# Performance work log

Measured on AMD Instinct MI355X. Metric: run time of the kernel, lower is better.

Reference implementation:

```python
import jax, jax.numpy as jnp
import numpy as np

VOCAB, D = 32000, 1024
EPS = 1e-5

def setup_inputs() -> dict:
    key = jax.random.key(0)
    k1, k2, k3, k4 = jax.random.split(key, 4)
    patch_embeddings = jax.random.normal(k1, (16, 256, D), dtype=jnp.float32)
    text_prototypes = jax.random.normal(k2, (VOCAB, D), dtype=jnp.float32) * 0.02
    # nn.Linear(d, d): weight [d, d], bias [d]
    lim = 1.0 / np.sqrt(D)
    W = jax.random.uniform(k3, (D, D), minval=-lim, maxval=lim, dtype=jnp.float32)
    b = jax.random.uniform(k4, (D,), minval=-lim, maxval=lim, dtype=jnp.float32)
    gamma = jnp.ones((D,), dtype=jnp.float32)
    beta = jnp.zeros((D,), dtype=jnp.float32)
    return {"patch_embeddings": patch_embeddings, "text_prototypes": text_prototypes,
            "W": W, "b": b, "gamma": gamma, "beta": beta}

def _layer_norm(x, gamma, beta):
    mu = jnp.mean(x, axis=-1, keepdims=True)
    var = jnp.mean(jnp.square(x - mu), axis=-1, keepdims=True)
    return (x - mu) * jax.lax.rsqrt(var + EPS) * gamma + beta

def reference(patch_embeddings, text_prototypes, W, b, gamma, beta):
    # similarities: [B, P, V]
    sims = jnp.einsum('bpd,vd->bpv', patch_embeddings, text_prototypes)
    attn = jax.nn.softmax(sims, axis=-1)
    reprogrammed = jnp.einsum('bpv,vd->bpd', attn, text_prototypes)
    transformed = jnp.einsum('bpd,ed->bpe', reprogrammed, W) + b
    return _layer_norm(patch_embeddings + transformed, gamma, beta)
```

## Files before the change

kernel.cpp:

```cpp
#include <hip/hip_runtime.h>
#include <hip/hip_bf16.h>
#include <cstdint>
#include <cstddef>

#define D_DIM 1024
#define VOCAB 32000
#define ROWS  4096

typedef __attribute__((ext_vector_type(8))) short bf16x8;
typedef __attribute__((ext_vector_type(4))) float f32x4;
typedef __attribute__((ext_vector_type(4))) int   i32x4;
typedef __attribute__((ext_vector_type(8))) int   i32x8;

static __device__ __forceinline__ i32x8 cat8(i32x4 lo, i32x4 hi) {
  return __builtin_shufflevector(lo, hi, 0, 1, 2, 3, 4, 5, 6, 7);
}

static __device__ __forceinline__ unsigned short f2bf(float f) {
  union { float f; unsigned int u; } c; c.f = f;
  unsigned int u = c.u;
  u += 0x7fffu + ((u >> 16) & 1u);
  return (unsigned short)(u >> 16);
}

static __device__ __forceinline__ int pk8(float a, float b) {
  return __builtin_amdgcn_cvt_pk_fp8_f32(a, b, 0, false);
}

static __device__ __forceinline__ void gload_lds16(const void* g, void* s) {
  __builtin_amdgcn_global_load_lds(
      (const __attribute__((address_space(1))) uint32_t*)(g),
      (__attribute__((address_space(3))) uint32_t*)(s), 16, 0, 0);
}

__global__ void k_cvt(const float* __restrict__ src, short* __restrict__ dst, int n4) {
  int i = blockIdx.x * 256 + threadIdx.x;
  if (i < n4) {
    float4 v = *(const float4*)(src + (size_t)i * 4);
    ushort4 u;
    u.x = f2bf(v.x); u.y = f2bf(v.y); u.z = f2bf(v.z); u.w = f2bf(v.w);
    *(ushort4*)(dst + (size_t)i * 4) = u;
  }
}

__global__ void k_cvt_q8(const float* __restrict__ src, uint8_t* __restrict__ dst) {
  int i = blockIdx.x * 256 + threadIdx.x;
  float4 a = *(const float4*)(src + (size_t)i * 8);
  float4 b = *(const float4*)(src + (size_t)i * 8 + 4);
  uint2 o;
  o.x = (pk8(a.x, a.y) & 0xffff) | (pk8(a.z, a.w) << 16);
  o.y = (pk8(b.x, b.y) & 0xffff) | (pk8(b.z, b.w) << 16);
  *(uint2*)(dst + (size_t)i * 8) = o;
}

__global__ void k_prep_K8(const float* __restrict__ src, uint8_t* __restrict__ kb,
                          uint8_t* __restrict__ kt, int R, int C) {
  __shared__ uint8_t tile[64][68];
  int t  = threadIdx.x;
  int r0 = blockIdx.x * 64;
  int c0 = blockIdx.y * 64;
  int lr = t >> 4;
  int lc = (t & 15) * 4;
#pragma unroll
  for (int i = 0; i < 4; ++i) {
    int r = lr + 16 * i;
    float4 v = *(const float4*)(src + (size_t)(r0 + r) * C + c0 + lc);
    unsigned p = (pk8(v.x * 64.f, v.y * 64.f) & 0xffff) | (pk8(v.z * 64.f, v.w * 64.f) << 16);
    *(unsigned*)&tile[r][lc] = p;
    *(unsigned*)(kb + (size_t)(r0 + r) * C + c0 + lc) = p;
  }
  __syncthreads();
#pragma unroll
  for (int i = 0; i < 4; ++i) {
    int c = lr + 16 * i;
    unsigned p = tile[lc + 0][c] | (tile[lc + 1][c] << 8) |
                 (tile[lc + 2][c] << 16) | ((unsigned)tile[lc + 3][c] << 24);
    *(unsigned*)(kt + (size_t)(c0 + c) * R + r0 + lc) = p;
  }
}

#define PS1 272
#define G1NT 8
__global__ __launch_bounds__(512, 1) void k_g1(
    const uint8_t* __restrict__ A,
    const uint8_t* __restrict__ B,
    uint8_t* __restrict__ Pout, float* __restrict__ den)
{
  __shared__ uint8_t smem[147456];

  int tid  = threadIdx.x;
  int wave = tid >> 6;
  int lane = tid & 63;
  int quad = lane >> 4;
  int t16  = lane & 15;
  int wm = wave >> 2;
  int wn = wave & 3;

  int swz = (blockIdx.x & 7) * 500 + (blockIdx.x >> 3);
  int nt  = swz >> 5;
  int mt  = swz & 31;
  long mBase = (long)mt * 128;
  long nBase = (long)nt * 256;

  const uint8_t* Ab = A + (size_t)mBase * D_DIM;
  const uint8_t* Bb = B + (size_t)nBase * D_DIM;
  int lrow = lane >> 3;
  int lcol = ((lane & 7) ^ lrow) * 16;

  f32x4 acc[4][4];
#pragma unroll
  for (int i = 0; i < 4; ++i)
#pragma unroll
    for (int j = 0; j < 4; ++j) acc[i][j] = (f32x4){0.f, 0.f, 0.f, 0.f};

  int sw  = t16 & 7;
  int co0 = (((quad << 1) ^ sw) << 4);
  const int SC1 = 0x7F7F7F7F;

  auto STAGE = [&](int slot, int t) {
    uint8_t* As = &smem[slot * 49152];
    uint8_t* Bs = As + 16384;
    int kk = t * 128;
#pragma unroll
    for (int g = 0; g < 2; ++g) {
      int r0 = wave * 16 + g * 8;
      gload_lds16(Ab + (size_t)(r0 + lrow) * D_DIM + kk + lcol, As + r0 * 128);
    }
#pragma unroll
    for (int g = 0; g < 4; ++g) {
      int r0 = wave * 32 + g * 8;
      gload_lds16(Bb + (size_t)(r0 + lrow) * D_DIM + kk + lcol, Bs + r0 * 128);
    }
  };

  STAGE(0, 0);
  STAGE(1, 1);

  for (int t = 0; t < G1NT; ++t) {
    if (t + 1 < G1NT)
      asm volatile("s_waitcnt vmcnt(6)\n\ts_barrier" ::: "memory");
    else
      asm volatile("s_waitcnt vmcnt(0)\n\ts_barrier" ::: "memory");

    if (t + 2 < G1NT) STAGE((t + 2) % 3, t + 2);

    const uint8_t* As = &smem[(t % 3) * 49152];
    const uint8_t* Bs = As + 16384;
    i32x8 af[4], bfr[4];
#pragma unroll
    for (int mi = 0; mi < 4; ++mi) {
      const uint8_t* rp = &As[(wm * 64 + mi * 16 + t16) * 128];
      af[mi] = cat8(*(const i32x4*)(rp + co0), *(const i32x4*)(rp + (co0 ^ 16)));
    }
#pragma unroll
    for (int ni = 0; ni < 4; ++ni) {
      const uint8_t* rp = &Bs[(wn * 64 + ni * 16 + t16) * 128];
      bfr[ni] = cat8(*(const i32x4*)(rp + co0), *(const i32x4*)(rp + (co0 ^ 16)));
    }
    __builtin_amdgcn_s_setprio(1);
#pragma unroll
    for (int mi = 0; mi < 4; ++mi)
#pragma unroll
      for (int ni = 0; ni < 4; ++ni)
        acc[mi][ni] = __builtin_amdgcn_mfma_scale_f32_16x16x128_f8f6f4(
            af[mi], bfr[ni], acc[mi][ni], 0, 0, 0, SC1, 0, SC1);
    __builtin_amdgcn_s_setprio(0);
  }

  __syncthreads();
  float rsum[4][4];
#pragma unroll
  for (int mi = 0; mi < 4; ++mi)
#pragma unroll
    for (int r = 0; r < 4; ++r) rsum[mi][r] = 0.f;
#pragma unroll
  for (int mi = 0; mi < 4; ++mi) {
    int rloc = wm * 64 + mi * 16 + quad * 4;
#pragma unroll
    for (int ni = 0; ni < 4; ++ni) {
      int cloc = wn * 64 + ni * 16 + t16;
#pragma unroll
      for (int r = 0; r < 4; ++r) {
        float e = __expf(acc[mi][ni][r] * 0.015625f);
        smem[(rloc + r) * PS1 + cloc] = (uint8_t)pk8(e, e);
        rsum[mi][r] += e;
      }
    }
  }
#pragma unroll
  for (int mi = 0; mi < 4; ++mi)
#pragma unroll
    for (int r = 0; r < 4; ++r) {
      float s = rsum[mi][r];
      s += __shfl_xor(s, 1);
      s += __shfl_xor(s, 2);
      s += __shfl_xor(s, 4);
      s += __shfl_xor(s, 8);
      if (t16 == 0)
        atomicAdd(&den[mBase + wm * 64 + mi * 16 + quad * 4 + r], s);
    }
  __syncthreads();
  int rr  = tid >> 4;
  int c16 = (tid & 15) * 16;
#pragma unroll
  for (int i = 0; i < 4; ++i) {
    int row = i * 32 + rr;
    i32x4 v = *(const i32x4*)&smem[row * PS1 + c16];
    __builtin_nontemporal_store(v, (i32x4*)&Pout[(size_t)(mBase + row) * VOCAB + nBase + c16]);
  }
}

#define G2NT 125
__global__ __launch_bounds__(512, 1) void k_g2(
    const uint8_t* __restrict__ P, const uint8_t* __restrict__ KT,
    float* __restrict__ n0, float* __restrict__ n1)
{
  __shared__ uint8_t smem[147456];

  int tid  = threadIdx.x;
  int wave = tid >> 6;
  int lane = tid & 63;
  int quad = lane >> 4;
  int t16  = lane & 15;
  int wm = wave >> 2;
  int wn = wave & 3;

  int bid = blockIdx.x;
  int dt  = bid & 3;
  int zz  = (bid >> 2) & 1;
  int mt  = bid >> 3;
  long mBase = (long)mt * 128;
  long dBase = (long)dt * 256;
  int  k0    = zz * 16000;

  const uint8_t* Ab = P  + (size_t)mBase * VOCAB + k0;
  const uint8_t* Bb = KT + (size_t)dBase * VOCAB + k0;
  int lrow = lane >> 3;
  int lcol = ((lane & 7) ^ lrow) * 16;

  f32x4 acc[4][4];
#pragma unroll
  for (int i = 0; i < 4; ++i)
#pragma unroll
    for (int j = 0; j < 4; ++j) acc[i][j] = (f32x4){0.f, 0.f, 0.f, 0.f};

  int sw  = t16 & 7;
  int co0 = (((quad << 1) ^ sw) << 4);
  const int SC1 = 0x7F7F7F7F;

  auto STAGE = [&](int slot, int t) {
    uint8_t* As = &smem[slot * 49152];
    uint8_t* Bs = As + 16384;
    long kk = (long)t * 128;
#pragma unroll
    for (int g = 0; g < 2; ++g) {
      int r0 = wave * 16 + g * 8;
      gload_lds16(Ab + (size_t)(r0 + lrow) * VOCAB + kk + lcol, As + r0 * 128);
    }
#pragma unroll
    for (int g = 0; g < 4; ++g) {
      int r0 = wave * 32 + g * 8;
      gload_lds16(Bb + (size_t)(r0 + lrow) * VOCAB + kk + lcol, Bs + r0 * 128);
    }
  };

  STAGE(0, 0);
  STAGE(1, 1);

  for (int t = 0; t < G2NT; ++t) {
    if (t + 1 < G2NT)
      asm volatile("s_waitcnt vmcnt(6)\n\ts_barrier" ::: "memory");
    else
      asm volatile("s_waitcnt vmcnt(0)\n\ts_barrier" ::: "memory");

    if (t + 2 < G2NT) STAGE((t + 2) % 3, t + 2);

    const uint8_t* As = &smem[(t % 3) * 49152];
    const uint8_t* Bs = As + 16384;
    i32x8 af[4], bfr[4];
#pragma unroll
    for (int mi = 0; mi < 4; ++mi) {
      const uint8_t* rp = &As[(wm * 64 + mi * 16 + t16) * 128];
      af[mi] = cat8(*(const i32x4*)(rp + co0), *(const i32x4*)(rp + (co0 ^ 16)));
    }
#pragma unroll
    for (int ni = 0; ni < 4; ++ni) {
      const uint8_t* rp = &Bs[(wn * 64 + ni * 16 + t16) * 128];
      bfr[ni] = cat8(*(const i32x4*)(rp + co0), *(const i32x4*)(rp + (co0 ^ 16)));
    }
    __builtin_amdgcn_s_setprio(1);
#pragma unroll
    for (int mi = 0; mi < 4; ++mi)
#pragma unroll
      for (int ni = 0; ni < 4; ++ni)
        acc[mi][ni] = __builtin_amdgcn_mfma_scale_f32_16x16x128_f8f6f4(
            af[mi], bfr[ni], acc[mi][ni], 0, 0, 0, SC1, 0, SC1);
    __builtin_amdgcn_s_setprio(0);
  }

  float* outp = zz ? n1 : n0;
#pragma unroll
  for (int mi = 0; mi < 4; ++mi) {
    long row = mBase + wm * 64 + mi * 16 + quad * 4;
#pragma unroll
    for (int ni = 0; ni < 4; ++ni) {
      long col = dBase + wn * 64 + ni * 16 + t16;
#pragma unroll
      for (int r = 0; r < 4; ++r)
        outp[(size_t)(row + r) * D_DIM + col] = acc[mi][ni][r];
    }
  }
}

__global__ __launch_bounds__(256) void k_gemm_bf(
    const short* __restrict__ A, int lda,
    const short* __restrict__ B, int ldb, int Kdim,
    const float* __restrict__ bias, const float* __restrict__ resid,
    float* __restrict__ Cout)
{
  __shared__ short smem[16384];
  short* As = smem;
  short* Bs = smem + 8192;

  int tid  = threadIdx.x;
  int wave = tid >> 6;
  int lane = tid & 63;
  int quad = lane >> 4;
  int t16  = lane & 15;
  int wy = wave >> 1, wx = wave & 1;

  long mBase = (long)blockIdx.y * 128;
  long nBase = (long)blockIdx.x * 128;

  const short* Ab = A + (size_t)mBase * lda;
  const short* Bb = B + (size_t)nBase * ldb;
  int lrow = lane >> 3;
  int lcol = ((lane & 7) ^ lrow) * 8;

  f32x4 acc[4][4];
#pragma unroll
  for (int i = 0; i < 4; ++i)
#pragma unroll
    for (int j = 0; j < 4; ++j) acc[i][j] = (f32x4){0.f, 0.f, 0.f, 0.f};

  int sw = t16 & 7;

  for (int kk = 0; kk < Kdim; kk += 64) {
#pragma unroll
    for (int i = 0; i < 4; ++i) {
      int row = wave * 32 + i * 8;
      gload_lds16(Ab + (size_t)(row + lrow) * lda + kk + lcol, &As[row * 64]);
      gload_lds16(Bb + (size_t)(row + lrow) * ldb + kk + lcol, &Bs[row * 64]);
    }
    __syncthreads();
#pragma unroll
    for (int kc = 0; kc < 8; kc += 4) {
      bf16x8 af[4], bfr[4];
#pragma unroll
      for (int mi = 0; mi < 4; ++mi)
        af[mi] = *(const bf16x8*)&As[(wy * 64 + mi * 16 + t16) * 64 +
                                     (((kc + quad) ^ sw) << 3)];
#pragma unroll
      for (int ni = 0; ni < 4; ++ni)
        bfr[ni] = *(const bf16x8*)&Bs[(wx * 64 + ni * 16 + t16) * 64 +
                                      (((kc + quad) ^ sw) << 3)];
#pragma unroll
      for (int mi = 0; mi < 4; ++mi)
#pragma unroll
        for (int ni = 0; ni < 4; ++ni)
          acc[mi][ni] = __builtin_amdgcn_mfma_f32_16x16x32_bf16(af[mi], bfr[ni],
                                                                acc[mi][ni], 0, 0, 0);
    }
    __syncthreads();
  }

#pragma unroll
  for (int mi = 0; mi < 4; ++mi) {
    long row = mBase + wy * 64 + mi * 16 + quad * 4;
#pragma unroll
    for (int ni = 0; ni < 4; ++ni) {
      long col = nBase + wx * 64 + ni * 16 + t16;
#pragma unroll
      for (int r = 0; r < 4; ++r) {
        size_t idx = (size_t)(row + r) * 1024 + col;
        Cout[idx] = acc[mi][ni][r] + bias[col] + resid[idx];
      }
    }
  }
}

__global__ void k_div(const float* __restrict__ n0, const float* __restrict__ n1,
                      const float* __restrict__ den, short* __restrict__ out) {
  int i = (blockIdx.x * 256 + threadIdx.x) * 4;
  float4 a = *(const float4*)(n0 + i);
  float4 b = *(const float4*)(n1 + i);
  float inv = 0.015625f / den[i >> 10];
  ushort4 u;
  u.x = f2bf((a.x + b.x) * inv); u.y = f2bf((a.y + b.y) * inv);
  u.z = f2bf((a.z + b.z) * inv); u.w = f2bf((a.w + b.w) * inv);
  *(ushort4*)(out + i) = u;
}

__global__ __launch_bounds__(256) void k_ln(const float* __restrict__ x,
                                            const float* __restrict__ gamma,
                                            const float* __restrict__ beta,
                                            float* __restrict__ out) {
  __shared__ float s_sum[4], s_sq[4];
  int row = blockIdx.x;
  int tid = threadIdx.x;
  const float* xr = x + (size_t)row * 1024;
  float4 v = *(const float4*)(xr + tid * 4);
  float s = v.x + v.y + v.z + v.w;
  float q = v.x * v.x + v.y * v.y + v.z * v.z + v.w * v.w;
#pragma unroll
  for (int off = 32; off >= 1; off >>= 1) {
    s += __shfl_down(s, off);
    q += __shfl_down(q, off);
  }
  int wv = tid >> 6;
  if ((tid & 63) == 0) { s_sum[wv] = s; s_sq[wv] = q; }
  __syncthreads();
  float tot  = s_sum[0] + s_sum[1] + s_sum[2] + s_sum[3];
  float totq = s_sq[0] + s_sq[1] + s_sq[2] + s_sq[3];
  float mu   = tot * (1.0f / 1024.0f);
  float var  = totq * (1.0f / 1024.0f) - mu * mu;
  float rstd = rsqrtf(var + 1e-5f);
  float4 g = *(const float4*)(gamma + tid * 4);
  float4 b = *(const float4*)(beta + tid * 4);
  float4 o;
  o.x = (v.x - mu) * rstd * g.x + b.x;
  o.y = (v.y - mu) * rstd * g.y + b.y;
  o.z = (v.z - mu) * rstd * g.z + b.z;
  o.w = (v.w - mu) * rstd * g.w + b.w;
  *(float4*)(out + (size_t)row * 1024 + tid * 4) = o;
}

extern "C" void kernel_launch(void* const* d_in, const int* in_sizes, int n_in,
                              void* d_out, int out_size, void* d_ws, size_t ws_size,
                              hipStream_t stream) {
  const float* patch = (const float*)d_in[0];
  const float* proto = (const float*)d_in[1];
  const float* W     = (const float*)d_in[2];
  const float* bvec  = (const float*)d_in[3];
  const float* gamma = (const float*)d_in[4];
  const float* beta  = (const float*)d_in[5];
  float* out = (float*)d_out;

  char* ws = (char*)d_ws;
  size_t off = 0;
  uint8_t* Q8  = (uint8_t*)(ws + off); off += (size_t)ROWS * D_DIM;
  uint8_t* Kb8 = (uint8_t*)(ws + off); off += (size_t)VOCAB * D_DIM;
  uint8_t* KT8 = (uint8_t*)(ws + off); off += (size_t)VOCAB * D_DIM;
  short*   Wb  = (short*)(ws + off);   off += (size_t)D_DIM * D_DIM * 2;
  short*   Rb  = (short*)(ws + off);   off += (size_t)ROWS * D_DIM * 2;
  uint8_t* P8  = (uint8_t*)(ws + off); off += (size_t)ROWS * VOCAB;
  float*   num = (float*)(ws + off);   off += (size_t)ROWS * D_DIM * 4;
  float*   den = (float*)(ws + off);   off += (size_t)ROWS * 4;
  float*   pre = (float*)P8;
  float*   nz0 = (float*)Kb8;
  float*   nz1 = num;

  hipMemsetAsync(den, 0, ROWS * sizeof(float), stream);

  k_cvt_q8<<<ROWS * D_DIM / 8 / 256, 256, 0, stream>>>(patch, Q8);
  k_cvt<<<D_DIM * D_DIM / 4 / 256, 256, 0, stream>>>(W, Wb, D_DIM * D_DIM / 4);
  k_prep_K8<<<dim3(VOCAB / 64, D_DIM / 64), 256, 0, stream>>>(proto, Kb8, KT8, VOCAB, D_DIM);

  k_g1<<<4000, 512, 0, stream>>>(Q8, Kb8, P8, den);

  k_g2<<<256, 512, 0, stream>>>(P8, KT8, nz0, nz1);

  k_div<<<ROWS * D_DIM / 4 / 256, 256, 0, stream>>>(nz0, nz1, den, Rb);

  k_gemm_bf<<<dim3(D_DIM / 128, ROWS / 128), 256, 0, stream>>>(
      Rb, D_DIM, Wb, D_DIM, D_DIM, bvec, patch, pre);

  k_ln<<<ROWS, 256, 0, stream>>>(pre, gamma, beta, out);
}
```

Before: 634.9 us.

## Enlarge GEMM tiles to 256x256, double-buffer, and split g2 K five ways

Both fp8 GEMM kernels move from 128x256 to 256x256 block tiles with 8 MFMA column fragments per wave, which raises data reuse per LDS load. The K loop changes from a triple-buffered to a double-buffered LDS pipeline, with an explicit barrier before each refill. The second GEMM now splits K into five chunks over 320 blocks instead of two chunks over 256, to fill the GPU better. Four of the chunks accumulate through float atomics into buffers that are zeroed by an extra memset, and the divide kernel sums three partial buffers. The cost is more accumulator registers, atomic traffic, the extra memset and a shallower prefetch.

```diff
diff --git a/kernel.cpp b/kernel.cpp
--- a/kernel.cpp
+++ b/kernel.cpp
@@ -81,25 +81,25 @@
 
 #define PS1 272
 #define G1NT 8
-__global__ __launch_bounds__(512, 1) void k_g1(
+__global__ __launch_bounds__(512, 2) void k_g1(
     const uint8_t* __restrict__ A,
     const uint8_t* __restrict__ B,
     uint8_t* __restrict__ Pout, float* __restrict__ den)
 {
-  __shared__ uint8_t smem[147456];
+  __shared__ uint8_t smem[131072];
 
   int tid  = threadIdx.x;
   int wave = tid >> 6;
   int lane = tid & 63;
   int quad = lane >> 4;
   int t16  = lane & 15;
-  int wm = wave >> 2;
-  int wn = wave & 3;
-
-  int swz = (blockIdx.x & 7) * 500 + (blockIdx.x >> 3);
-  int nt  = swz >> 5;
-  int mt  = swz & 31;
-  long mBase = (long)mt * 128;
+  int wm = wave >> 1;
+  int wn = wave & 1;
+
+  int swz = (blockIdx.x & 7) * 250 + (blockIdx.x >> 3);
+  int nt  = swz >> 4;
+  int mt  = swz & 15;
+  long mBase = (long)mt * 256;
   long nBase = (long)nt * 256;
 
   const uint8_t* Ab = A + (size_t)mBase * D_DIM;
@@ -107,23 +107,23 @@
   int lrow = lane >> 3;
   int lcol = ((lane & 7) ^ lrow) * 16;
 
-  f32x4 acc[4][4];
+  f32x4 acc[4][8];
 #pragma unroll
   for (int i = 0; i < 4; ++i)
 #pragma unroll
-    for (int j = 0; j < 4; ++j) acc[i][j] = (f32x4){0.f, 0.f, 0.f, 0.f};
+    for (int j = 0; j < 8; ++j) acc[i][j] = (f32x4){0.f, 0.f, 0.f, 0.f};
 
   int sw  = t16 & 7;
   int co0 = (((quad << 1) ^ sw) << 4);
   const int SC1 = 0x7F7F7F7F;
 
   auto STAGE = [&](int slot, int t) {
-    uint8_t* As = &smem[slot * 49152];
-    uint8_t* Bs = As + 16384;
+    uint8_t* As = &smem[slot * 65536];
+    uint8_t* Bs = As + 32768;
     int kk = t * 128;
 #pragma unroll
-    for (int g = 0; g < 2; ++g) {
-      int r0 = wave * 16 + g * 8;
+    for (int g = 0; g < 4; ++g) {
+      int r0 = wave * 32 + g * 8;
       gload_lds16(Ab + (size_t)(r0 + lrow) * D_DIM + kk + lcol, As + r0 * 128);
     }
 #pragma unroll
@@ -138,36 +138,34 @@
 
   for (int t = 0; t < G1NT; ++t) {
     if (t + 1 < G1NT)
-      asm volatile("s_waitcnt vmcnt(6)\n\ts_barrier" ::: "memory");
+      asm volatile("s_waitcnt vmcnt(8)\n\ts_barrier" ::: "memory");
     else
       asm volatile("s_waitcnt vmcnt(0)\n\ts_barrier" ::: "memory");
 
-    if (t + 2 < G1NT) STAGE((t + 2) % 3, t + 2);
-
-    const uint8_t* As = &smem[(t % 3) * 49152];
-    const uint8_t* Bs = As + 16384;
-    i32x8 af[4], bfr[4];
+    const uint8_t* As = &smem[(t & 1) * 65536];
+    const uint8_t* Bs = As + 32768;
+
+    i32x8 bf[8];
+#pragma unroll
+    for (int ni = 0; ni < 8; ++ni) {
+      const uint8_t* rp = &Bs[(wn * 128 + ni * 16 + t16) * 128];
+      bf[ni] = cat8(*(const i32x4*)(rp + co0), *(const i32x4*)(rp + (co0 ^ 16)));
+    }
+    __builtin_amdgcn_s_setprio(1);
 #pragma unroll
     for (int mi = 0; mi < 4; ++mi) {
       const uint8_t* rp = &As[(wm * 64 + mi * 16 + t16) * 128];
-      af[mi] = cat8(*(const i32x4*)(rp + co0), *(const i32x4*)(rp + (co0 ^ 16)));
-    }
-#pragma unroll
-    for (int ni = 0; ni < 4; ++ni) {
-      const uint8_t* rp = &Bs[(wn * 64 + ni * 16 + t16) * 128];
-      bfr[ni] = cat8(*(const i32x4*)(rp + co0), *(const i32x4*)(rp + (co0 ^ 16)));
-    }
-    __builtin_amdgcn_s_setprio(1);
-#pragma unroll
-    for (int mi = 0; mi < 4; ++mi)
-#pragma unroll
-      for (int ni = 0; ni < 4; ++ni)
+      i32x8 am = cat8(*(const i32x4*)(rp + co0), *(const i32x4*)(rp + (co0 ^ 16)));
+#pragma unroll
+      for (int ni = 0; ni < 8; ++ni)
         acc[mi][ni] = __builtin_amdgcn_mfma_scale_f32_16x16x128_f8f6f4(
-            af[mi], bfr[ni], acc[mi][ni], 0, 0, 0, SC1, 0, SC1);
+            am, bf[ni], acc[mi][ni], 0, 0, 0, SC1, 0, SC1);
+    }
     __builtin_amdgcn_s_setprio(0);
-  }
-
-  __syncthreads();
+    asm volatile("s_barrier" ::: "memory");
+    if (t + 2 < G1NT) STAGE(t & 1, t + 2);
+  }
+
   float rsum[4][4];
 #pragma unroll
   for (int mi = 0; mi < 4; ++mi)
@@ -177,8 +175,8 @@
   for (int mi = 0; mi < 4; ++mi) {
     int rloc = wm * 64 + mi * 16 + quad * 4;
 #pragma unroll
-    for (int ni = 0; ni < 4; ++ni) {
-      int cloc = wn * 64 + ni * 16 + t16;
+    for (int ni = 0; ni < 8; ++ni) {
+      int cloc = wn * 128 + ni * 16 + t16;
 #pragma unroll
       for (int r = 0; r < 4; ++r) {
         float e = __expf(acc[mi][ni][r] * 0.015625f);
@@ -203,58 +201,58 @@
   int rr  = tid >> 4;
   int c16 = (tid & 15) * 16;
 #pragma unroll
-  for (int i = 0; i < 4; ++i) {
+  for (int i = 0; i < 8; ++i) {
     int row = i * 32 + rr;
     i32x4 v = *(const i32x4*)&smem[row * PS1 + c16];
     __builtin_nontemporal_store(v, (i32x4*)&Pout[(size_t)(mBase + row) * VOCAB + nBase + c16]);
   }
 }
 
-#define G2NT 125
-__global__ __launch_bounds__(512, 1) void k_g2(
+#define G2NT 50
+__global__ __launch_bounds__(512, 2) void k_g2(
     const uint8_t* __restrict__ P, const uint8_t* __restrict__ KT,
-    float* __restrict__ n0, float* __restrict__ n1)
+    float* __restrict__ s0, float* __restrict__ s1, float* __restrict__ s2)
 {
-  __shared__ uint8_t smem[147456];
+  __shared__ uint8_t smem[131072];
 
   int tid  = threadIdx.x;
   int wave = tid >> 6;
   int lane = tid & 63;
   int quad = lane >> 4;
   int t16  = lane & 15;
-  int wm = wave >> 2;
-  int wn = wave & 3;
+  int wm = wave >> 1;
+  int wn = wave & 1;
 
   int bid = blockIdx.x;
   int dt  = bid & 3;
-  int zz  = (bid >> 2) & 1;
-  int mt  = bid >> 3;
-  long mBase = (long)mt * 128;
+  int mt  = (bid >> 2) & 15;
+  int zz  = bid >> 6;
+  long mBase = (long)mt * 256;
   long dBase = (long)dt * 256;
-  int  k0    = zz * 16000;
+  int  k0    = zz * 6400;
 
   const uint8_t* Ab = P  + (size_t)mBase * VOCAB + k0;
   const uint8_t* Bb = KT + (size_t)dBase * VOCAB + k0;
   int lrow = lane >> 3;
   int lcol = ((lane & 7) ^ lrow) * 16;
 
-  f32x4 acc[4][4];
+  f32x4 acc[4][8];
 #pragma unroll
   for (int i = 0; i < 4; ++i)
 #pragma unroll
-    for (int j = 0; j < 4; ++j) acc[i][j] = (f32x4){0.f, 0.f, 0.f, 0.f};
+    for (int j = 0; j < 8; ++j) acc[i][j] = (f32x4){0.f, 0.f, 0.f, 0.f};
 
   int sw  = t16 & 7;
   int co0 = (((quad << 1) ^ sw) << 4);
   const int SC1 = 0x7F7F7F7F;
 
   auto STAGE = [&](int slot, int t) {
-    uint8_t* As = &smem[slot * 49152];
-    uint8_t* Bs = As + 16384;
+    uint8_t* As = &smem[slot * 65536];
+    uint8_t* Bs = As + 32768;
     long kk = (long)t * 128;
 #pragma unroll
-    for (int g = 0; g < 2; ++g) {
-      int r0 = wave * 16 + g * 8;
+    for (int g = 0; g < 4; ++g) {
+      int r0 = wave * 32 + g * 8;
       gload_lds16(Ab + (size_t)(r0 + lrow) * VOCAB + kk + lcol, As + r0 * 128);
     }
 #pragma unroll
@@ -269,45 +267,48 @@
 
   for (int t = 0; t < G2NT; ++t) {
     if (t + 1 < G2NT)
-      asm volatile("s_waitcnt vmcnt(6)\n\ts_barrier" ::: "memory");
+      asm volatile("s_waitcnt vmcnt(8)\n\ts_barrier" ::: "memory");
     else
       asm volatile("s_waitcnt vmcnt(0)\n\ts_barrier" ::: "memory");
 
-    if (t + 2 < G2NT) STAGE((t + 2) % 3, t + 2);
-
-    const uint8_t* As = &smem[(t % 3) * 49152];
-    const uint8_t* Bs = As + 16384;
-    i32x8 af[4], bfr[4];
+    const uint8_t* As = &smem[(t & 1) * 65536];
+    const uint8_t* Bs = As + 32768;
+
+    i32x8 bf[8];
+#pragma unroll
+    for (int ni = 0; ni < 8; ++ni) {
+      const uint8_t* rp = &Bs[(wn * 128 + ni * 16 + t16) * 128];
+      bf[ni] = cat8(*(const i32x4*)(rp + co0), *(const i32x4*)(rp + (co0 ^ 16)));
+    }
+    __builtin_amdgcn_s_setprio(1);
 #pragma unroll
     for (int mi = 0; mi < 4; ++mi) {
       const uint8_t* rp = &As[(wm * 64 + mi * 16 + t16) * 128];
-      af[mi] = cat8(*(const i32x4*)(rp + co0), *(const i32x4*)(rp + (co0 ^ 16)));
-    }
-#pragma unroll
-    for (int ni = 0; ni < 4; ++ni) {
-      const uint8_t* rp = &Bs[(wn * 64 + ni * 16 + t16) * 128];
-      bfr[ni] = cat8(*(const i32x4*)(rp + co0), *(const i32x4*)(rp + (co0 ^ 16)));
-    }
-    __builtin_amdgcn_s_setprio(1);
-#pragma unroll
-    for (int mi = 0; mi < 4; ++mi)
-#pragma unroll
-      for (int ni = 0; ni < 4; ++ni)
+      i32x8 am = cat8(*(const i32x4*)(rp + co0), *(const i32x4*)(rp + (co0 ^ 16)));
+#pragma unroll
+      for (int ni = 0; ni < 8; ++ni)
         acc[mi][ni] = __builtin_amdgcn_mfma_scale_f32_16x16x128_f8f6f4(
-            af[mi], bfr[ni], acc[mi][ni], 0, 0, 0, SC1, 0, SC1);
+            am, bf[ni], acc[mi][ni], 0, 0, 0, SC1, 0, SC1);
+    }
     __builtin_amdgcn_s_setprio(0);
-  }
-
-  float* outp = zz ? n1 : n0;
+    asm volatile("s_barrier" ::: "memory");
+    if (t + 2 < G2NT) STAGE(t & 1, t + 2);
+  }
+
+  float* outp = (zz == 2) ? s2 : ((zz == 0 || zz == 3) ? s0 : s1);
+  bool plain = (zz == 2);
 #pragma unroll
   for (int mi = 0; mi < 4; ++mi) {
     long row = mBase + wm * 64 + mi * 16 + quad * 4;
 #pragma unroll
-    for (int ni = 0; ni < 4; ++ni) {
-      long col = dBase + wn * 64 + ni * 16 + t16;
-#pragma unroll
-      for (int r = 0; r < 4; ++r)
-        outp[(size_t)(row + r) * D_DIM + col] = acc[mi][ni][r];
+    for (int ni = 0; ni < 8; ++ni) {
+      long col = dBase + wn * 128 + ni * 16 + t16;
+#pragma unroll
+      for (int r = 0; r < 4; ++r) {
+        float* p = &outp[(size_t)(row + r) * D_DIM + col];
+        if (plain) *p = acc[mi][ni][r];
+        else       atomicAdd(p, acc[mi][ni][r]);
+      }
     }
   }
 }
@@ -389,15 +390,17 @@
   }
 }
 
-__global__ void k_div(const float* __restrict__ n0, const float* __restrict__ n1,
+__global__ void k_div(const float* __restrict__ s0, const float* __restrict__ s1,
+                      const float* __restrict__ s2,
                       const float* __restrict__ den, short* __restrict__ out) {
   int i = (blockIdx.x * 256 + threadIdx.x) * 4;
-  float4 a = *(const float4*)(n0 + i);
-  float4 b = *(const float4*)(n1 + i);
+  float4 a = *(const float4*)(s0 + i);
+  float4 b = *(const float4*)(s1 + i);
+  float4 c = *(const float4*)(s2 + i);
   float inv = 0.015625f / den[i >> 10];
   ushort4 u;
-  u.x = f2bf((a.x + b.x) * inv); u.y = f2bf((a.y + b.y) * inv);
-  u.z = f2bf((a.z + b.z) * inv); u.w = f2bf((a.w + b.w) * inv);
+  u.x = f2bf((a.x + b.x + c.x) * inv); u.y = f2bf((a.y + b.y + c.y) * inv);
+  u.z = f2bf((a.z + b.z + c.z) * inv); u.w = f2bf((a.w + b.w + c.w) * inv);
   *(ushort4*)(out + i) = u;
 }
 
@@ -457,8 +460,9 @@
   float*   num = (float*)(ws + off);   off += (size_t)ROWS * D_DIM * 4;
   float*   den = (float*)(ws + off);   off += (size_t)ROWS * 4;
   float*   pre = (float*)P8;
-  float*   nz0 = (float*)Kb8;
-  float*   nz1 = num;
+  float*   sz0 = (float*)(ws);
+  float*   sz1 = (float*)(ws + (size_t)16 * 1024 * 1024);
+  float*   sz2 = num;
 
   hipMemsetAsync(den, 0, ROWS * sizeof(float), stream);
 
@@ -466,11 +470,13 @@
   k_cvt<<<D_DIM * D_DIM / 4 / 256, 256, 0, stream>>>(W, Wb, D_DIM * D_DIM / 4);
   k_prep_K8<<<dim3(VOCAB / 64, D_DIM / 64), 256, 0, stream>>>(proto, Kb8, KT8, VOCAB, D_DIM);
 
-  k_g1<<<4000, 512, 0, stream>>>(Q8, Kb8, P8, den);
-
-  k_g2<<<256, 512, 0, stream>>>(P8, KT8, nz0, nz1);
-
-  k_div<<<ROWS * D_DIM / 4 / 256, 256, 0, stream>>>(nz0, nz1, den, Rb);
+  k_g1<<<2000, 512, 0, stream>>>(Q8, Kb8, P8, den);
+
+  hipMemsetAsync(sz0, 0, (size_t)32 * 1024 * 1024, stream);
+
+  k_g2<<<320, 512, 0, stream>>>(P8, KT8, sz0, sz1, sz2);
+
+  k_div<<<ROWS * D_DIM / 4 / 256, 256, 0, stream>>>(sz0, sz1, sz2, den, Rb);
 
   k_gemm_bf<<<dim3(D_DIM / 128, ROWS / 128), 256, 0, stream>>>(
       Rb, D_DIM, Wb, D_DIM, D_DIM, bvec, patch, pre);
```

New measurement: 862.1 us. +35.8%, slower.
